# Optimization experiments

Measured on AMD Instinct MI355X. Metric: run time of the kernel, lower is better.

Reference implementation:

```python
import jax, jax.numpy as jnp
import numpy as np

B, C, H, W, RED = 32, 128, 32, 32, 8
CR = C // RED


def pw(w, x):
    # 1x1 conv as channel contraction: w [O,Cin], x [B,Cin,H,W]
    return jnp.einsum('oc,bchw->bohw', w, x)


def dw(x, k):
    # depthwise 3x3, SAME padding; k [C,1,3,3]
    return jax.lax.conv_general_dilated(
        x, k, (1, 1), 'SAME', feature_group_count=C,
        dimension_numbers=('NCHW', 'OIHW', 'NCHW'))


def setup_inputs() -> dict:
    key = jax.random.key(0)
    ks = jax.random.split(key, 32)
    s = 0.05
    d = {
        'h_t': jax.random.normal(ks[0], (B, C, H, W), jnp.float32),
        'm_prev': jax.random.normal(ks[1], (B, C, H, W), jnp.float32),
        'wq_h': jax.random.normal(ks[2], (CR, C)) * s,
        'wk_h': jax.random.normal(ks[3], (CR, C)) * s,
        'wv_h': jax.random.normal(ks[4], (C, C)) * s,
        'wk_m': jax.random.normal(ks[5], (CR, C)) * s,
        'wv_m': jax.random.normal(ks[6], (C, C)) * s,
        'wz_w': jax.random.normal(ks[7], (C, 2 * C)) * s,
        'wz_b': jnp.zeros((C,)),
        'wmi_dw': jax.random.normal(ks[8], (C, 1, 3, 3)) * s,
        'wmi_pw': jax.random.normal(ks[9], (C, C)) * s,
        'whi_dw': jax.random.normal(ks[10], (C, 1, 3, 3)) * s,
        'whi_pw': jax.random.normal(ks[11], (C, C)) * s,
        'bi': jnp.zeros((C,)),
        'wmg_dw': jax.random.normal(ks[12], (C, 1, 3, 3)) * s,
        'wmg_pw': jax.random.normal(ks[13], (C, C)) * s,
        'whg_dw': jax.random.normal(ks[14], (C, 1, 3, 3)) * s,
        'whg_pw': jax.random.normal(ks[15], (C, C)) * s,
        'bg': jnp.zeros((C,)),
        'wmo_dw': jax.random.normal(ks[16], (C, 1, 3, 3)) * s,
        'wmo_pw': jax.random.normal(ks[17], (C, C)) * s,
        'who_dw': jax.random.normal(ks[18], (C, 1, 3, 3)) * s,
        'who_pw': jax.random.normal(ks[19], (C, C)) * s,
        'bo': jnp.zeros((C,)),
        'wf_w': jax.random.normal(ks[20], (C, C)) * s,
        'wf_b': jnp.zeros((C,)),
    }
    return d


def reference(h_t, m_prev, wq_h, wk_h, wv_h, wk_m, wv_m, wz_w, wz_b,
              wmi_dw, wmi_pw, whi_dw, whi_pw, bi,
              wmg_dw, wmg_pw, whg_dw, whg_pw, bg,
              wmo_dw, wmo_pw, who_dw, who_pw, bo, wf_w, wf_b):
    b, c, h, w = h_t.shape
    N = h * w
    # shared-Q dual attention; Q/K are [B,Cr,N], V are [B,C,N]
    Q = pw(wq_h, h_t).reshape(b, -1, N)
    K_h = pw(wk_h, h_t).reshape(b, -1, N)
    V_h = pw(wv_h, h_t).reshape(b, c, N)
    attn_h = jax.nn.softmax(jnp.einsum('bki,bkj->bij', Q, K_h), axis=-1)  # [B,N,N]
    Z_h = jnp.einsum('bcj,bij->bci', V_h, attn_h).reshape(b, c, h, w)
    K_m = pw(wk_m, m_prev).reshape(b, -1, N)
    V_m = pw(wv_m, m_prev).reshape(b, c, N)
    attn_m = jax.nn.softmax(jnp.einsum('bki,bkj->bij', Q, K_m), axis=-1)
    Z_m = jnp.einsum('bcj,bij->bci', V_m, attn_m).reshape(b, c, h, w)
    Z = pw(wz_w, jnp.concatenate([Z_h, Z_m], axis=1)) + wz_b[None, :, None, None]
    # ConvLSTM-style gated fusion (depthwise 3x3 + pointwise 1x1 pairs)
    i_t = jax.nn.sigmoid(pw(wmi_pw, dw(Z, wmi_dw)) + pw(whi_pw, dw(h_t, whi_dw)) + bi[None, :, None, None])
    g_t = jnp.tanh(pw(wmg_pw, dw(Z, wmg_dw)) + pw(whg_pw, dw(h_t, whg_dw)) + bg[None, :, None, None])
    m_t = (1 - i_t) * m_prev + i_t * g_t
    o_t = jax.nn.sigmoid(pw(wmo_pw, dw(Z, wmo_dw)) + pw(who_pw, dw(h_t, who_dw)) + bo[None, :, None, None])
    h_out = o_t * m_t
    h_out = pw(wf_w, h_out) + wf_b[None, :, None, None] + h_t
    return (h_out, m_t)
```

## Files before the change

### kernel.cpp

```cpp
#include <hip/hip_runtime.h>
#include <hip/hip_bf16.h>
#include <math.h>

#define BB   32
#define CCH  128
#define NPIX 1024
#define CRED 16

typedef __attribute__((ext_vector_type(8)))  short short8;
typedef __attribute__((ext_vector_type(16))) float f32x16;

union Frag8 { short8 s8; unsigned u[4]; };

__device__ __forceinline__ unsigned pack2bf(float lo, float hi) {
    union { __hip_bfloat16 h; unsigned short u; } a, b;
    a.h = __float2bfloat16(lo);
    b.h = __float2bfloat16(hi);
    return (unsigned)a.u | ((unsigned)b.u << 16);
}

__global__ __launch_bounds__(256)
void wcvt_kernel(__hip_bfloat16* __restrict__ dst,
                 const float* __restrict__ s0, const float* __restrict__ s1,
                 const float* __restrict__ wz,
                 const float* __restrict__ s4, const float* __restrict__ s5,
                 const float* __restrict__ s6, const float* __restrict__ s7,
                 const float* __restrict__ s8, const float* __restrict__ s9,
                 const float* __restrict__ s10)
{
    const int slot = blockIdx.y;
    const int e = (blockIdx.x * 256 + threadIdx.x) * 4;
    const float* src;
    size_t soff;
    if (slot == 2 || slot == 3) {
        const int o = e >> 7, c = e & 127;
        src = wz;
        soff = (size_t)o * 256 + (slot == 3 ? 128 : 0) + c;
    } else {
        switch (slot) {
            case 0: src = s0; break;  case 1: src = s1; break;
            case 4: src = s4; break;  case 5: src = s5; break;
            case 6: src = s6; break;  case 7: src = s7; break;
            case 8: src = s8; break;  case 9: src = s9; break;
            default: src = s10; break;
        }
        soff = e;
    }
    float4 v = *(const float4*)&src[soff];
    uint2 pk = make_uint2(pack2bf(v.x, v.y), pack2bf(v.z, v.w));
    *(uint2*)&dst[(size_t)slot * 16384 + e] = pk;
}

__device__ __forceinline__ void stage_tile(char* buf, const float* Xb, int tid)
{
    const int p  = tid & 63;
    const int gb = tid >> 6;
    float xr[32];
    #pragma unroll
    for (int u = 0; u < 8; ++u) {
        const int c0 = (u * 4 + gb) * 4;
        #pragma unroll
        for (int j = 0; j < 4; ++j)
            xr[u * 4 + j] = Xb[(size_t)(c0 + j) * NPIX + p];
    }
    #pragma unroll
    for (int u = 0; u < 8; ++u) {
        const int g = u * 4 + gb;
        uint2 pk = make_uint2(pack2bf(xr[u * 4 + 0], xr[u * 4 + 1]),
                              pack2bf(xr[u * 4 + 2], xr[u * 4 + 3]));
        *(uint2*)(buf + p * 256 + ((g ^ (p & 31)) << 3)) = pk;
    }
}

__device__ __forceinline__ void stage_tile_bf16(char* buf,
                                                const __hip_bfloat16* Xb, int tid)
{
    const unsigned short* Xu = (const unsigned short*)Xb;
    const int p  = tid & 63;
    const int gb = tid >> 6;
    #pragma unroll
    for (int u = 0; u < 8; ++u) {
        const int g  = u * 4 + gb;
        const int c0 = g * 4;
        unsigned e0 = Xu[(size_t)(c0 + 0) * NPIX + p];
        unsigned e1 = Xu[(size_t)(c0 + 1) * NPIX + p];
        unsigned e2 = Xu[(size_t)(c0 + 2) * NPIX + p];
        unsigned e3 = Xu[(size_t)(c0 + 3) * NPIX + p];
        uint2 pk = make_uint2(e0 | (e1 << 16), e2 | (e3 << 16));
        *(uint2*)(buf + p * 256 + ((g ^ (p & 31)) << 3)) = pk;
    }
}

__device__ __forceinline__ void compute_pass(const char* buf,
                                             const __hip_bfloat16* W,
                                             f32x16* acc,
                                             int l31, int H, int ntw, int mth)
{
    const int prow = (32 * ntw + l31) * 256;
    #pragma unroll
    for (int kt = 0; kt < 8; ++kt) {
        Frag8 bf_;
        const int g0 = 4 * kt + 2 * H;
        *(uint2*)&bf_.u[0] = *(const uint2*)(buf + prow + (((g0    ) ^ l31) << 3));
        *(uint2*)&bf_.u[2] = *(const uint2*)(buf + prow + (((g0 + 1) ^ l31) << 3));
        #pragma unroll
        for (int mi = 0; mi < 2; ++mi) {
            const int m = 32 * (2 * mth + mi) + l31;
            short8 af = *(const short8*)&W[(size_t)m * 128 + 16 * kt + 8 * H];
            acc[mi] = __builtin_amdgcn_mfma_f32_32x32x16_bf16(af, bf_.s8, acc[mi], 0, 0, 0);
        }
    }
}

template<bool TWO, bool BF16IN, bool BF16OUT>
__global__ __launch_bounds__(256)
void pw_mfma(void* __restrict__ outv,
             const void* __restrict__ X1, const __hip_bfloat16* __restrict__ W1,
             const void* __restrict__ X2, const __hip_bfloat16* __restrict__ W2,
             const float* __restrict__ bias, const float* __restrict__ res)
{
    __shared__ __align__(16) char Xs[2][16384];
    const int tid = threadIdx.x;
    const int b   = blockIdx.y;
    const int p0  = blockIdx.x * 64;
    const int l31 = tid & 31;
    const int H   = (tid & 63) >> 5;
    const int w   = tid >> 6;
    const int ntw = w & 1;
    const int mth = w >> 1;
    const size_t boff = (size_t)b * CCH * NPIX + p0;

    if (BF16IN) stage_tile_bf16(&Xs[0][0], (const __hip_bfloat16*)X1 + boff, tid);
    else        stage_tile     (&Xs[0][0], (const float*)X1 + boff, tid);
    if (TWO) {
        if (BF16IN) stage_tile_bf16(&Xs[1][0], (const __hip_bfloat16*)X2 + boff, tid);
        else        stage_tile     (&Xs[1][0], (const float*)X2 + boff, tid);
    }
    __syncthreads();

    f32x16 acc[2];
    #pragma unroll
    for (int mi = 0; mi < 2; ++mi)
        #pragma unroll
        for (int e = 0; e < 16; ++e) acc[mi][e] = 0.f;

    compute_pass(&Xs[0][0], W1, acc, l31, H, ntw, mth);
    if (TWO)
        compute_pass(&Xs[1][0], W2, acc, l31, H, ntw, mth);

    const int pg = p0 + 32 * ntw + l31;
    #pragma unroll
    for (int mi = 0; mi < 2; ++mi) {
        const int mtile = 2 * mth + mi;
        #pragma unroll
        for (int r = 0; r < 16; ++r) {
            const int m = 32 * mtile + (r & 3) + 8 * (r >> 2) + 4 * H;
            float v = acc[mi][r];
            if (bias) v += bias[m];
            const size_t off = ((size_t)b * CCH + m) * NPIX + pg;
            if (res) v += res[off];
            if (BF16OUT) ((__hip_bfloat16*)outv)[off] = __float2bfloat16(v);
            else         ((float*)outv)[off] = v;
        }
    }
}

__global__ __launch_bounds__(256)
void qkproj_kernel(__hip_bfloat16* __restrict__ Qt,
                   __hip_bfloat16* __restrict__ Kht,
                   __hip_bfloat16* __restrict__ Kmt,
                   const float* __restrict__ h_t,
                   const float* __restrict__ m_prev,
                   const float* __restrict__ wq,
                   const float* __restrict__ wkh,
                   const float* __restrict__ wkm)
{
    const int b  = blockIdx.y;
    const int p0 = blockIdx.x * 128;
    const float* X; const float* W; __hip_bfloat16* Out;
    if (blockIdx.z == 0)      { X = h_t;    W = wq;  Out = Qt;  }
    else if (blockIdx.z == 1) { X = h_t;    W = wkh; Out = Kht; }
    else                      { X = m_prev; W = wkm; Out = Kmt; }

    __shared__ float Ws[16][128];
    __shared__ float Xs[32][132];
    const int tid = threadIdx.x;
    for (int i = tid; i < 16 * 128; i += 256)
        Ws[i / 128][i % 128] = W[i];

    const float* Xb = X + (size_t)b * CCH * NPIX;
    const int pl = tid & 127;
    const int h8 = tid >> 7;

    float acc[8];
    #pragma unroll
    for (int e = 0; e < 8; ++e) acc[e] = 0.f;

    for (int c0 = 0; c0 < CCH; c0 += 32) {
        __syncthreads();
        for (int idx = tid; idx < 32 * 32; idx += 256) {
            int r = idx >> 5, cp = (idx & 31) << 2;
            *(float4*)&Xs[r][cp] =
                *(const float4*)&Xb[(size_t)(c0 + r) * NPIX + p0 + cp];
        }
        __syncthreads();
        #pragma unroll 8
        for (int cc = 0; cc < 32; ++cc) {
            float xv = Xs[cc][pl];
            #pragma unroll
            for (int e = 0; e < 8; ++e)
                acc[e] += Ws[h8 * 8 + e][c0 + cc] * xv;
        }
    }

    Frag8 f;
    #pragma unroll
    for (int w = 0; w < 4; ++w)
        f.u[w] = pack2bf(acc[2 * w], acc[2 * w + 1]);
    *(short8*)&Out[((size_t)b * NPIX + p0 + pl) * 16 + 8 * h8] = f.s8;
}

__global__ __launch_bounds__(256)
void dw6_kernel(__hip_bfloat16* __restrict__ D, size_t SVe,
                const float* __restrict__ Z, const float* __restrict__ h_t,
                const float* __restrict__ wmi, const float* __restrict__ wmg,
                const float* __restrict__ wmo,
                const float* __restrict__ whi, const float* __restrict__ whg,
                const float* __restrict__ who)
{
    const int c = blockIdx.x, b = blockIdx.y;
    const float* src; const float *kaw, *kbw, *kcw;
    __hip_bfloat16* dbase;
    if (blockIdx.z == 0) { src = Z;   kaw = wmi; kbw = wmg; kcw = wmo; dbase = D; }
    else                 { src = h_t; kaw = whi; kbw = whg; kcw = who; dbase = D + 3 * SVe; }
    const size_t chan = ((size_t)b * CCH + c) * NPIX;
    src += chan;
    __hip_bfloat16* d0 = dbase + chan;
    __hip_bfloat16* d1 = d0 + SVe;
    __hip_bfloat16* d2 = d1 + SVe;

    float ka[9], kb[9], kc[9];
    #pragma unroll
    for (int j = 0; j < 9; ++j) {
        ka[j] = kaw[c * 9 + j];
        kb[j] = kbw[c * 9 + j];
        kc[j] = kcw[c * 9 + j];
    }

    __shared__ float t[34][36];
    const int tid = threadIdx.x;
    for (int idx = tid; idx < 34 * 34; idx += 256) {
        int y = idx / 34, x = idx % 34;
        int gy = y - 1, gx = x - 1;
        t[y][x] = (gy >= 0 && gy < 32 && gx >= 0 && gx < 32)
                      ? src[gy * 32 + gx] : 0.f;
    }
    __syncthreads();
    const int x = tid % 32, y0 = tid / 32;
    #pragma unroll
    for (int q = 0; q < 4; ++q) {
        int y = y0 + 8 * q;
        float s0 = 0.f, s1 = 0.f, s2 = 0.f;
        #pragma unroll
        for (int dy = 0; dy < 3; ++dy)
            #pragma unroll
            for (int dx = 0; dx < 3; ++dx) {
                float tv = t[y + dy][x + dx];
                s0 += tv * ka[dy * 3 + dx];
                s1 += tv * kb[dy * 3 + dx];
                s2 += tv * kc[dy * 3 + dx];
            }
        d0[y * 32 + x] = __float2bfloat16(s0);
        d1[y * 32 + x] = __float2bfloat16(s1);
        d2[y * 32 + x] = __float2bfloat16(s2);
    }
}

__global__ __launch_bounds__(256)
void gates_mfma(float* __restrict__ mt_out, float* __restrict__ om_out,
                const __hip_bfloat16* __restrict__ D, size_t SVe,
                const __hip_bfloat16* __restrict__ Wg,
                const float* __restrict__ bi, const float* __restrict__ bg,
                const float* __restrict__ bo, const float* __restrict__ mp)
{
    __shared__ __align__(16) char Xs[2][16384];
    const int tid = threadIdx.x;
    const int b   = blockIdx.y;
    const int p0  = blockIdx.x * 64;
    const int l31 = tid & 31;
    const int H   = (tid & 63) >> 5;
    const int w   = tid >> 6;
    const int ntw = w & 1;
    const int mth = w >> 1;
    const size_t boff = (size_t)b * CCH * NPIX + p0;

    const int ds[6] = {0, 3, 1, 4, 2, 5};

    f32x16 acc[6];
    #pragma unroll
    for (int a = 0; a < 6; ++a)
        #pragma unroll
        for (int e = 0; e < 16; ++e) acc[a][e] = 0.f;

    stage_tile_bf16(&Xs[0][0], D + (size_t)ds[0] * SVe + boff, tid);
    __syncthreads();

    #pragma unroll
    for (int s = 0; s < 6; ++s) {
        if (s < 5)
            stage_tile_bf16(&Xs[(s + 1) & 1][0], D + (size_t)ds[s + 1] * SVe + boff, tid);
        compute_pass(&Xs[s & 1][0], Wg + (size_t)s * 16384,
                     &acc[2 * (s >> 1)], l31, H, ntw, mth);
        __syncthreads();
    }

    const int pg = p0 + 32 * ntw + l31;
    #pragma unroll
    for (int mi = 0; mi < 2; ++mi) {
        const int mtile = 2 * mth + mi;
        #pragma unroll
        for (int r = 0; r < 16; ++r) {
            const int m = 32 * mtile + (r & 3) + 8 * (r >> 2) + 4 * H;
            const size_t off = ((size_t)b * CCH + m) * NPIX + pg;
            float it = 1.f / (1.f + __expf(-(acc[0 + mi][r] + bi[m])));
            float gt = tanhf(acc[2 + mi][r] + bg[m]);
            float ot = 1.f / (1.f + __expf(-(acc[4 + mi][r] + bo[m])));
            float mpv = mp[off];
            float mt = (1.f - it) * mpv + it * gt;
            mt_out[off] = mt;
            om_out[off] = ot * mt;
        }
    }
}

__global__ __launch_bounds__(256)
void attn_mfma_kernel(__hip_bfloat16* __restrict__ Zh,
                      __hip_bfloat16* __restrict__ Zm,
                      const __hip_bfloat16* __restrict__ Qt,
                      const __hip_bfloat16* __restrict__ Kht,
                      const __hip_bfloat16* __restrict__ Kmt,
                      const __hip_bfloat16* __restrict__ Vh,
                      const __hip_bfloat16* __restrict__ Vm)
{
    const int b  = blockIdx.y;
    const int i0 = blockIdx.x * 128;
    const __hip_bfloat16* Kt; const __hip_bfloat16* Vg; __hip_bfloat16* Og;
    if (blockIdx.z == 0) { Kt = Kht; Vg = Vh; Og = Zh; }
    else                 { Kt = Kmt; Vg = Vm; Og = Zm; }
    Kt += (size_t)b * NPIX * 16;
    Vg += (size_t)b * CCH * NPIX;
    Og += (size_t)b * CCH * NPIX;

    __shared__ __align__(16) char Vs[2][128 * 64 * 2];

    const int tid = threadIdx.x;
    const int w   = tid >> 6;
    const int l   = tid & 63;
    const int l31 = l & 31;
    const int H   = l >> 5;

    const __hip_bfloat16* Qb = Qt + (size_t)b * NPIX * 16;
    short8 qf = *(const short8*)&Qb[((size_t)(i0 + 32 * w + l31)) * 16 + 8 * H];

    f32x16 acc[4];
    #pragma unroll
    for (int ct = 0; ct < 4; ++ct)
        #pragma unroll
        for (int e = 0; e < 16; ++e) acc[ct][e] = 0.f;
    float l_acc = 0.f;

    int cu[4], ldsoff[4]; size_t goff[4];
    #pragma unroll
    for (int u = 0; u < 4; ++u) {
        int idx = tid + 256 * u;
        cu[u] = idx >> 3;
        int jg = idx & 7;
        ldsoff[u] = cu[u] * 128 + ((jg ^ (cu[u] & 7)) << 4);
        goff[u]   = (size_t)cu[u] * NPIX + 8 * jg;
    }
    const int slotx_base = (l31 & 7);

    short8 v0 = *(const short8*)&Vg[goff[0]];
    short8 v1 = *(const short8*)&Vg[goff[1]];
    short8 v2 = *(const short8*)&Vg[goff[2]];
    short8 v3 = *(const short8*)&Vg[goff[3]];
    short8 kf0 = *(const short8*)&Kt[(size_t)(0 + l31) * 16 + 8 * H];
    short8 kf1 = *(const short8*)&Kt[(size_t)(32 + l31) * 16 + 8 * H];

    for (int t = 0; t < 16; ++t) {
        char* buf = &Vs[t & 1][0];
        *(short8*)(buf + ldsoff[0]) = v0;
        *(short8*)(buf + ldsoff[1]) = v1;
        *(short8*)(buf + ldsoff[2]) = v2;
        *(short8*)(buf + ldsoff[3]) = v3;

        short8 kn0 = kf0, kn1 = kf1;
        if (t < 15) {
            const int jn = (t + 1) * 64;
            v0 = *(const short8*)&Vg[goff[0] + jn];
            v1 = *(const short8*)&Vg[goff[1] + jn];
            v2 = *(const short8*)&Vg[goff[2] + jn];
            v3 = *(const short8*)&Vg[goff[3] + jn];
            kn0 = *(const short8*)&Kt[(size_t)(jn + l31) * 16 + 8 * H];
            kn1 = *(const short8*)&Kt[(size_t)(jn + 32 + l31) * 16 + 8 * H];
        }
        __syncthreads();

        #pragma unroll
        for (int jt = 0; jt < 2; ++jt) {
            short8 kcur = (jt == 0) ? kf0 : kf1;
            f32x16 z;
            #pragma unroll
            for (int e = 0; e < 16; ++e) z[e] = 0.f;
            f32x16 s = __builtin_amdgcn_mfma_f32_32x32x16_bf16(kcur, qf, z, 0, 0, 0);

            float p[16];
            float ls = 0.f;
            #pragma unroll
            for (int r = 0; r < 16; ++r) { p[r] = __expf(s[r]); ls += p[r]; }
            l_acc += ls + __shfl_xor(ls, 32);

            unsigned w0[4], w1[4], x0[4], x1[4];
            #pragma unroll
            for (int g = 0; g < 4; ++g) {
                w0[g] = pack2bf(p[4 * g + 0], p[4 * g + 1]);
                w1[g] = pack2bf(p[4 * g + 2], p[4 * g + 3]);
            }
            #pragma unroll
            for (int g = 0; g < 4; ++g) {
                x0[g] = __shfl_xor(w0[g], 32);
                x1[g] = __shfl_xor(w1[g], 32);
            }
            #pragma unroll
            for (int js = 0; js < 2; ++js) {
                const int gA = 2 * js, gB = 2 * js + 1;
                Frag8 pb;
                pb.u[0] = H ? x0[gB] : w0[gA];
                pb.u[1] = H ? x1[gB] : w1[gA];
                pb.u[2] = H ? w0[gB] : x0[gA];
                pb.u[3] = H ? w1[gB] : x1[gA];
                const int slot = 4 * jt + 2 * js + H;
                const int sx   = (slot ^ slotx_base) << 4;
                #pragma unroll
                for (int ct = 0; ct < 4; ++ct) {
                    short8 vf = *(short8*)(buf + (32 * ct + l31) * 128 + sx);
                    acc[ct] = __builtin_amdgcn_mfma_f32_32x32x16_bf16(
                        vf, pb.s8, acc[ct], 0, 0, 0);
                }
            }
        }
        kf0 = kn0; kf1 = kn1;
    }

    const float linv = 1.0f / l_acc;
    const int ig = i0 + 32 * w + l31;
    #pragma unroll
    for (int ct = 0; ct < 4; ++ct) {
        #pragma unroll
        for (int r = 0; r < 16; ++r) {
            int c = 32 * ct + (r & 3) + 8 * (r >> 2) + 4 * H;
            Og[(size_t)c * NPIX + ig] = __float2bfloat16(acc[ct][r] * linv);
        }
    }
}

extern "C" void kernel_launch(void* const* d_in, const int* in_sizes, int n_in,
                              void* d_out, int out_size, void* d_ws, size_t ws_size,
                              hipStream_t stream)
{
    (void)in_sizes; (void)n_in; (void)out_size; (void)ws_size;
    const float* h_t    = (const float*)d_in[0];
    const float* m_prev = (const float*)d_in[1];
    const float* wq_h   = (const float*)d_in[2];
    const float* wk_h   = (const float*)d_in[3];
    const float* wv_h   = (const float*)d_in[4];
    const float* wk_m   = (const float*)d_in[5];
    const float* wv_m   = (const float*)d_in[6];
    const float* wz_w   = (const float*)d_in[7];
    const float* wz_b   = (const float*)d_in[8];
    const float* wmi_dw = (const float*)d_in[9];
    const float* wmi_pw = (const float*)d_in[10];
    const float* whi_dw = (const float*)d_in[11];
    const float* whi_pw = (const float*)d_in[12];
    const float* bi     = (const float*)d_in[13];
    const float* wmg_dw = (const float*)d_in[14];
    const float* wmg_pw = (const float*)d_in[15];
    const float* whg_dw = (const float*)d_in[16];
    const float* whg_pw = (const float*)d_in[17];
    const float* bg     = (const float*)d_in[18];
    const float* wmo_dw = (const float*)d_in[19];
    const float* wmo_pw = (const float*)d_in[20];
    const float* who_dw = (const float*)d_in[21];
    const float* who_pw = (const float*)d_in[22];
    const float* bo     = (const float*)d_in[23];
    const float* wf_w   = (const float*)d_in[24];
    const float* wf_b   = (const float*)d_in[25];

    float* out = (float*)d_out;

    const size_t SQE = (size_t)BB * NPIX * CRED;
    const size_t SV  = (size_t)BB * CCH * NPIX;

    __hip_bfloat16* Wb  = (__hip_bfloat16*)d_ws;
    __hip_bfloat16* Qt  = Wb + 184320;
    __hip_bfloat16* Kht = Qt  + SQE;
    __hip_bfloat16* Kmt = Kht + SQE;
    __hip_bfloat16* Vhb = Kmt + SQE;
    __hip_bfloat16* Vmb = Vhb + SV;
    __hip_bfloat16* Zhb = Vmb + SV;
    __hip_bfloat16* Zmb = Zhb + SV;
    __hip_bfloat16* Dd  = Zmb + SV;
    float* Ev = (float*)(Dd + 6 * SV);
    float* Fv = Ev + SV;

    dim3 blk(256);
    dim3 pwg(NPIX / 64, BB);

    wcvt_kernel<<<dim3(16, 11), blk, 0, stream>>>(
        Wb, wv_h, wv_m, wz_w, wmi_pw, whi_pw, wmg_pw, whg_pw, wmo_pw, who_pw, wf_w);

    qkproj_kernel<<<dim3(NPIX / 128, BB, 3), blk, 0, stream>>>(
        Qt, Kht, Kmt, h_t, m_prev, wq_h, wk_h, wk_m);
    pw_mfma<false, false, true><<<pwg, blk, 0, stream>>>(
        Vhb, h_t, Wb + 0 * 16384, nullptr, nullptr, nullptr, nullptr);
    pw_mfma<false, false, true><<<pwg, blk, 0, stream>>>(
        Vmb, m_prev, Wb + 1 * 16384, nullptr, nullptr, nullptr, nullptr);

    attn_mfma_kernel<<<dim3(NPIX / 128, BB, 2), blk, 0, stream>>>(
        Zhb, Zmb, Qt, Kht, Kmt, Vhb, Vmb);

    pw_mfma<true, true, false><<<pwg, blk, 0, stream>>>(
        Ev, Zhb, Wb + 2 * 16384, Zmb, Wb + 3 * 16384, wz_b, nullptr);

    dw6_kernel<<<dim3(CCH, BB, 2), blk, 0, stream>>>(
        Dd, SV, Ev, h_t, wmi_dw, wmg_dw, wmo_dw, whi_dw, whg_dw, who_dw);

    gates_mfma<<<pwg, blk, 0, stream>>>(
        out + SV, Fv, Dd, SV, Wb + 4 * 16384, bi, bg, bo, m_prev);

    pw_mfma<false, false, false><<<pwg, blk, 0, stream>>>(
        out, Fv, Wb + 10 * 16384, nullptr, nullptr, wf_b, h_t);
}
```

Measured before the change: 301.2 us.

## Fuse gate GEMMs with final projection, row-major depthwise output layout

The final 1x1 projection (wf) is folded into the gate kernel, so o_t*m_t no longer makes a round trip to global memory in fp32 and one launch disappears. The depthwise kernel now writes its bf16 outputs in a [B,row,C,32] layout. Each block of the new gates kernel handles one image row of 32 pixels and stages all six depthwise tiles into swizzled LDS at once. This trades fewer launches and less intermediate traffic for smaller N tiles per block (32 pixels instead of 64) and more LDS per block, which may lower MFMA efficiency and occupancy.

```diff
diff --git a/kernel.cpp b/kernel.cpp
--- a/kernel.cpp
+++ b/kernel.cpp
@@ -233,11 +233,7 @@
     __hip_bfloat16* dbase;
     if (blockIdx.z == 0) { src = Z;   kaw = wmi; kbw = wmg; kcw = wmo; dbase = D; }
     else                 { src = h_t; kaw = whi; kbw = whg; kcw = who; dbase = D + 3 * SVe; }
-    const size_t chan = ((size_t)b * CCH + c) * NPIX;
-    src += chan;
-    __hip_bfloat16* d0 = dbase + chan;
-    __hip_bfloat16* d1 = d0 + SVe;
-    __hip_bfloat16* d2 = d1 + SVe;
+    src += ((size_t)b * CCH + c) * NPIX;
 
     float ka[9], kb[9], kc[9];
     #pragma unroll
@@ -270,66 +266,124 @@
                 s1 += tv * kb[dy * 3 + dx];
                 s2 += tv * kc[dy * 3 + dx];
             }
-        d0[y * 32 + x] = __float2bfloat16(s0);
-        d1[y * 32 + x] = __float2bfloat16(s1);
-        d2[y * 32 + x] = __float2bfloat16(s2);
+        const size_t o = ((size_t)(b * 32 + y) * CCH + c) * 32 + x;
+        dbase[o]           = __float2bfloat16(s0);
+        dbase[SVe + o]     = __float2bfloat16(s1);
+        dbase[2 * SVe + o] = __float2bfloat16(s2);
+    }
+}
+
+__device__ __forceinline__ void pass32(const char* buf,
+                                       const __hip_bfloat16* W,
+                                       f32x16* acc, int l31, int H, int wv)
+{
+    const int prow = l31 * 256;
+    #pragma unroll
+    for (int kt = 0; kt < 8; ++kt) {
+        Frag8 bf_;
+        const int g0 = 4 * kt + 2 * H;
+        *(uint2*)&bf_.u[0] = *(const uint2*)(buf + prow + (((g0    ) ^ l31) << 3));
+        *(uint2*)&bf_.u[2] = *(const uint2*)(buf + prow + (((g0 + 1) ^ l31) << 3));
+        const int m = 32 * wv + l31;
+        short8 af = *(const short8*)&W[(size_t)m * 128 + 16 * kt + 8 * H];
+        *acc = __builtin_amdgcn_mfma_f32_32x32x16_bf16(af, bf_.s8, *acc, 0, 0, 0);
     }
 }
 
 __global__ __launch_bounds__(256)
-void gates_mfma(float* __restrict__ mt_out, float* __restrict__ om_out,
-                const __hip_bfloat16* __restrict__ D, size_t SVe,
-                const __hip_bfloat16* __restrict__ Wg,
-                const float* __restrict__ bi, const float* __restrict__ bg,
-                const float* __restrict__ bo, const float* __restrict__ mp)
-{
-    __shared__ __align__(16) char Xs[2][16384];
+void gates3_kernel(float* __restrict__ mt_out, float* __restrict__ hout,
+                   const __hip_bfloat16* __restrict__ D, size_t SVe,
+                   const __hip_bfloat16* __restrict__ Wg,
+                   const __hip_bfloat16* __restrict__ Wf,
+                   const float* __restrict__ bi, const float* __restrict__ bg,
+                   const float* __restrict__ bo, const float* __restrict__ wfb,
+                   const float* __restrict__ mp, const float* __restrict__ h_t)
+{
+    __shared__ __align__(16) char Xs[6][8192];
     const int tid = threadIdx.x;
+    const int y   = blockIdx.x;
     const int b   = blockIdx.y;
-    const int p0  = blockIdx.x * 64;
     const int l31 = tid & 31;
     const int H   = (tid & 63) >> 5;
-    const int w   = tid >> 6;
-    const int ntw = w & 1;
-    const int mth = w >> 1;
-    const size_t boff = (size_t)b * CCH * NPIX + p0;
-
-    const int ds[6] = {0, 3, 1, 4, 2, 5};
-
-    f32x16 acc[6];
-    #pragma unroll
-    for (int a = 0; a < 6; ++a)
-        #pragma unroll
-        for (int e = 0; e < 16; ++e) acc[a][e] = 0.f;
-
-    stage_tile_bf16(&Xs[0][0], D + (size_t)ds[0] * SVe + boff, tid);
+    const int wv  = tid >> 6;
+    const size_t tbase = (size_t)(b * 32 + y) * 4096;
+
+    const int cs = tid >> 1;
+    const int ph = (tid & 1) << 4;
+    const int gs = cs >> 2;
+    const int cb = (cs & 3) << 1;
+    #pragma unroll
+    for (int s = 0; s < 6; ++s) {
+        const unsigned short* src =
+            (const unsigned short*)(D + (size_t)s * SVe + tbase + cs * 32 + ph);
+        short8 va = *(const short8*)(src);
+        short8 vb = *(const short8*)(src + 8);
+        char* buf = &Xs[s][0];
+        #pragma unroll
+        for (int j = 0; j < 8; ++j) {
+            const int pa = ph + j, pb2 = ph + 8 + j;
+            *(unsigned short*)(buf + pa  * 256 + ((gs ^ pa)  << 3) + cb) =
+                (unsigned short)va[j];
+            *(unsigned short*)(buf + pb2 * 256 + ((gs ^ pb2) << 3) + cb) =
+                (unsigned short)vb[j];
+        }
+    }
+
+    const int pg = (y << 5) + l31;
+    float mpv[16];
+    #pragma unroll
+    for (int r = 0; r < 16; ++r) {
+        const int m = 32 * wv + (r & 3) + 8 * (r >> 2) + 4 * H;
+        mpv[r] = mp[((size_t)b * CCH + m) * NPIX + pg];
+    }
+
     __syncthreads();
 
-    #pragma unroll
-    for (int s = 0; s < 6; ++s) {
-        if (s < 5)
-            stage_tile_bf16(&Xs[(s + 1) & 1][0], D + (size_t)ds[s + 1] * SVe + boff, tid);
-        compute_pass(&Xs[s & 1][0], Wg + (size_t)s * 16384,
-                     &acc[2 * (s >> 1)], l31, H, ntw, mth);
-        __syncthreads();
-    }
-
-    const int pg = p0 + 32 * ntw + l31;
-    #pragma unroll
-    for (int mi = 0; mi < 2; ++mi) {
-        const int mtile = 2 * mth + mi;
-        #pragma unroll
-        for (int r = 0; r < 16; ++r) {
-            const int m = 32 * mtile + (r & 3) + 8 * (r >> 2) + 4 * H;
-            const size_t off = ((size_t)b * CCH + m) * NPIX + pg;
-            float it = 1.f / (1.f + __expf(-(acc[0 + mi][r] + bi[m])));
-            float gt = tanhf(acc[2 + mi][r] + bg[m]);
-            float ot = 1.f / (1.f + __expf(-(acc[4 + mi][r] + bo[m])));
-            float mpv = mp[off];
-            float mt = (1.f - it) * mpv + it * gt;
-            mt_out[off] = mt;
-            om_out[off] = ot * mt;
-        }
+    f32x16 aI, aG, aO;
+    #pragma unroll
+    for (int e = 0; e < 16; ++e) { aI[e] = 0.f; aG[e] = 0.f; aO[e] = 0.f; }
+
+    pass32(&Xs[0][0], Wg + 0 * 16384, &aI, l31, H, wv);
+    pass32(&Xs[3][0], Wg + 1 * 16384, &aI, l31, H, wv);
+    pass32(&Xs[1][0], Wg + 2 * 16384, &aG, l31, H, wv);
+    pass32(&Xs[4][0], Wg + 3 * 16384, &aG, l31, H, wv);
+    pass32(&Xs[2][0], Wg + 4 * 16384, &aO, l31, H, wv);
+    pass32(&Xs[5][0], Wg + 5 * 16384, &aO, l31, H, wv);
+
+    float om[16];
+    #pragma unroll
+    for (int r = 0; r < 16; ++r) {
+        const int m = 32 * wv + (r & 3) + 8 * (r >> 2) + 4 * H;
+        const size_t off = ((size_t)b * CCH + m) * NPIX + pg;
+        float it = 1.f / (1.f + __expf(-(aI[r] + bi[m])));
+        float gt = tanhf(aG[r] + bg[m]);
+        float ot = 1.f / (1.f + __expf(-(aO[r] + bo[m])));
+        float mpv_r = mpv[r];
+        float mt = (1.f - it) * mpv_r + it * gt;
+        mt_out[off] = mt;
+        om[r] = ot * mt;
+    }
+
+    __syncthreads();
+    #pragma unroll
+    for (int q = 0; q < 4; ++q) {
+        const int g = 8 * wv + 2 * q + H;
+        uint2 pk = make_uint2(pack2bf(om[4 * q + 0], om[4 * q + 1]),
+                              pack2bf(om[4 * q + 2], om[4 * q + 3]));
+        *(uint2*)(&Xs[0][0] + l31 * 256 + ((g ^ l31) << 3)) = pk;
+    }
+    __syncthreads();
+
+    f32x16 aF;
+    #pragma unroll
+    for (int e = 0; e < 16; ++e) aF[e] = 0.f;
+    pass32(&Xs[0][0], Wf, &aF, l31, H, wv);
+
+    #pragma unroll
+    for (int r = 0; r < 16; ++r) {
+        const int m = 32 * wv + (r & 3) + 8 * (r >> 2) + 4 * H;
+        const size_t off = ((size_t)b * CCH + m) * NPIX + pg;
+        hout[off] = aF[r] + wfb[m] + h_t[off];
     }
 }
 
@@ -511,7 +565,6 @@
     __hip_bfloat16* Zmb = Zhb + SV;
     __hip_bfloat16* Dd  = Zmb + SV;
     float* Ev = (float*)(Dd + 6 * SV);
-    float* Fv = Ev + SV;
 
     dim3 blk(256);
     dim3 pwg(NPIX / 64, BB);
@@ -535,9 +588,7 @@
     dw6_kernel<<<dim3(CCH, BB, 2), blk, 0, stream>>>(
         Dd, SV, Ev, h_t, wmi_dw, wmg_dw, wmo_dw, whi_dw, whg_dw, who_dw);
 
-    gates_mfma<<<pwg, blk, 0, stream>>>(
-        out + SV, Fv, Dd, SV, Wb + 4 * 16384, bi, bg, bo, m_prev);
-
-    pw_mfma<false, false, false><<<pwg, blk, 0, stream>>>(
-        out, Fv, Wb + 10 * 16384, nullptr, nullptr, wf_b, h_t);
-}
+    gates3_kernel<<<dim3(32, BB), blk, 0, stream>>>(
+        out + SV, out, Dd, SV, Wb + 4 * 16384, Wb + 10 * 16384,
+        bi, bg, bo, wf_b, m_prev, h_t);
+}
```

New measurement: 288.5 us. -4.2%, faster.
